# Kernel optimization log

Hardware: AMD Instinct MI355X
Metric: run time of the kernel (lower is better)

## Reference

```python
import jax, jax.numpy as jnp
import numpy as np

K = 128      # classes
CIN = 128    # ch_in
CL = 128     # ch_latent
B, H, W = 8, 1, 8192
SLOPE = 0.01 # F.leaky_relu default
EPS = 1e-5   # BatchNorm eps


def lrelu(x):
    return jnp.where(x >= 0, x, SLOPE * x)


def conv1x1(x, w, b):
    # x: (B,C,H,W), w: (O,C), b: (O,)
    return jnp.einsum('bchw,oc->bohw', x, w) + b[None, :, None, None]


def bn_eval(x, gamma, beta, mean, var):
    scale = gamma * jax.lax.rsqrt(var + EPS)
    return x * scale[None, :, None, None] + (beta - mean * scale)[None, :, None, None]


def setup_inputs() -> dict:
    key = jax.random.key(0)
    ks = jax.random.split(key, 16)
    def w(k, shape, fan_in):
        return jax.random.normal(k, shape, jnp.float32) / np.sqrt(fan_in)
    return {
        'x_in': jax.random.normal(ks[0], (B, CIN, H, W), jnp.float32),
        'cl1_w': w(ks[1], (CL, CIN), CIN), 'cl1_b': jnp.zeros((CL,), jnp.float32),
        'bn1_gamma': jnp.ones((CL,), jnp.float32), 'bn1_beta': jnp.zeros((CL,), jnp.float32),
        'bn1_mean': 0.1 * jax.random.normal(ks[2], (CL,), jnp.float32),
        'bn1_var': jax.random.uniform(ks[3], (CL,), jnp.float32, 0.5, 1.5),
        'cl2_w': w(ks[4], (CL, CL), CL), 'cl2_b': jnp.zeros((CL,), jnp.float32),
        'cl3_w': w(ks[5], (K + 1, CL), CL), 'cl3_b': jnp.zeros((K + 1,), jnp.float32),
        'reg1_w': w(ks[6], (CL, CIN), CIN), 'reg1_b': jnp.zeros((CL,), jnp.float32),
        'bnr_gamma': jnp.ones((CL,), jnp.float32), 'bnr_beta': jnp.zeros((CL,), jnp.float32),
        'bnr_mean': 0.1 * jax.random.normal(ks[7], (CL,), jnp.float32),
        'bnr_var': jax.random.uniform(ks[8], (CL,), jnp.float32, 0.5, 1.5),
        'cm2_w': w(ks[9], (K, CL, 32), CL), 'cm2_b': jnp.zeros((K, 32), jnp.float32),
        'cm3_w': w(ks[10], (K, 32, 1), 32), 'cm3_b': jnp.zeros((K, 1), jnp.float32),
    }


def reference(x_in, cl1_w, cl1_b, bn1_gamma, bn1_beta, bn1_mean, bn1_var,
              cl2_w, cl2_b, cl3_w, cl3_b,
              reg1_w, reg1_b, bnr_gamma, bnr_beta, bnr_mean, bnr_var,
              cm2_w, cm2_b, cm3_w, cm3_b):
    # classification branch
    x = lrelu(bn_eval(conv1x1(x_in, cl1_w, cl1_b), bn1_gamma, bn1_beta, bn1_mean, bn1_var))
    x = lrelu(conv1x1(x, cl2_w, cl2_b))
    x = conv1x1(x, cl3_w, cl3_b)                    # (B, K+1, H, W)
    logits = x[:, :K]
    mask = lrelu(x[:, -1:])                          # (B,1,H,W)
    inds = jnp.argmax(logits, axis=1)                # (B,H,W) int
    inds_r = inds.reshape(-1).astype(jnp.int32)      # (N,)
    xr = lrelu(bn_eval(conv1x1(x_in, reg1_w, reg1_b), bnr_gamma, bnr_beta, bnr_mean, bnr_var))
    # torch: transpose(1,3).reshape(-1, C)  -> (B,W,H,C) flatten
    xr = jnp.transpose(xr, (0, 3, 2, 1)).reshape(-1, CL)   # (N, CL)
    # CondMul 1: per-pixel gathered weight (N,CL,32)
    h = lrelu(jnp.einsum('ni,nio->no', xr, cm2_w[inds_r]) + cm2_b[inds_r])
    # CondMul 2: (N,32)->(N,1)
    reg = jnp.einsum('ni,nio->no', h, cm3_w[inds_r]) + cm3_b[inds_r]
    reg = reg.reshape(B, 1, 1, -1)                   # (B,1,1,H*W)
    x_real = (inds[:, None].astype(jnp.float32) + reg) * (1.0 / K)
    return x_real, mask
```

## Files before the change

### kernel.cpp

```cpp
#include <hip/hip_runtime.h>
#include <math.h>

#define NPOS 65536
#define NCH  128
#define DELTA 0.008f
#define HPAD 16

#define OFF_XR   0u
#define OFF_W1T  8388608u
#define OFF_W2T  (OFF_W1T + 16384u)
#define OFF_W3T  (OFF_W2T + 16384u)
#define OFF_B1F  (OFF_W3T + 16384u)
#define OFF_BRF  (OFF_B1F + 128u)
#define OFF_B2F  (OFF_BRF + 128u)
#define OFF_B3F  (OFF_B2F + 128u)
#define OFF_BF16 (OFF_B3F + 132u)
#define OFF_INT  (OFF_BF16 + 329728u)

#define UW1H 0u
#define UW1L 16384u
#define UWRH 32768u
#define UWRL 49152u
#define UW2H 65536u
#define UW2L 81920u
#define UW3H 98304u
#define UW3L 116736u
#define UW2K 135168u

#define NST 2080

typedef short bf16x8 __attribute__((ext_vector_type(8)));
typedef float f32x4 __attribute__((ext_vector_type(4)));
#define MFMA16 __builtin_amdgcn_mfma_f32_16x16x32_bf16

__device__ __forceinline__ float lrelu(float v) { return v >= 0.0f ? v : 0.01f * v; }
__device__ __forceinline__ unsigned short f2bf(float f) {
    unsigned u = __float_as_uint(f);
    return (unsigned short)((u + 0x7fffu + ((u >> 16) & 1u)) >> 16);
}
__device__ __forceinline__ float bf2f(unsigned short h) {
    return __uint_as_float(((unsigned)h) << 16);
}
__device__ __forceinline__ unsigned long long pack4(unsigned short a, unsigned short b,
                                                    unsigned short c, unsigned short d) {
    return (unsigned long long)a | ((unsigned long long)b << 16)
         | ((unsigned long long)c << 32) | ((unsigned long long)d << 48);
}

__global__ void k_prep(const float* __restrict__ cl1_w, const float* __restrict__ cl1_b,
                       const float* __restrict__ g1, const float* __restrict__ be1,
                       const float* __restrict__ mu1, const float* __restrict__ va1,
                       const float* __restrict__ cl2_w, const float* __restrict__ cl2_b,
                       const float* __restrict__ cl3_w, const float* __restrict__ cl3_b,
                       const float* __restrict__ reg1_w, const float* __restrict__ reg1_b,
                       const float* __restrict__ gr, const float* __restrict__ ber,
                       const float* __restrict__ mur, const float* __restrict__ var_,
                       const float* __restrict__ cm2w,
                       float* __restrict__ ws_f, unsigned short* __restrict__ wbf,
                       int* __restrict__ hist, int* __restrict__ cur,
                       int* __restrict__ fixcnt)
{
    const int bid = blockIdx.x;
    const int t = threadIdx.x;
    if (bid >= 128) {
        __shared__ float tl[32 * 132];
        int k = bid - 128;
        #pragma unroll
        for (int i = 0; i < 32; ++i) {
            float v = cm2w[(unsigned)k * 4096u + i * 128 + t];
            int ci = i * 4 + (t >> 5), o = t & 31;
            tl[o * 132 + ci] = v;
        }
        __syncthreads();
        #pragma unroll
        for (int i = 0; i < 32; ++i)
            wbf[UW2K + (unsigned)k * 4096u + i * 128 + t] = f2bf(tl[i * 132 + t]);
        return;
    }
    const int cout = bid;
    const int cin = t;
    const int row = cout * 128 + cin;
    float s1 = g1[cout] / sqrtf(va1[cout] + 1e-5f);
    float sr = gr[cout] / sqrtf(var_[cout] + 1e-5f);
    float w1 = cl1_w[row] * s1;
    float wr = reg1_w[row] * sr;
    float w2 = cl2_w[row];
    float w3 = cl3_w[row];
    ws_f[OFF_W1T + cin * 128 + cout] = w1;
    ws_f[OFF_W2T + cin * 128 + cout] = w2;
    ws_f[OFF_W3T + cin * 128 + cout] = w3;
    unsigned short h;
    h = f2bf(w1); wbf[UW1H + row] = h; wbf[UW1L + row] = f2bf(w1 - bf2f(h));
    h = f2bf(wr); wbf[UWRH + row] = h; wbf[UWRL + row] = f2bf(wr - bf2f(h));
    h = f2bf(w2); wbf[UW2H + row] = h; wbf[UW2L + row] = f2bf(w2 - bf2f(h));
    h = f2bf(w3); wbf[UW3H + row] = h; wbf[UW3L + row] = f2bf(w3 - bf2f(h));
    if (bid < 16) {
        float v = (bid == 0) ? cl3_w[128 * 128 + t] : 0.0f;
        int jj = (128 + bid) * 128 + t;
        h = f2bf(v); wbf[UW3H + jj] = h; wbf[UW3L + jj] = f2bf(v - bf2f(h));
    }
    if (bid == 0) {
        float s1b = g1[t] / sqrtf(va1[t] + 1e-5f);
        float srb = gr[t] / sqrtf(var_[t] + 1e-5f);
        ws_f[OFF_B1F + t] = cl1_b[t] * s1b + be1[t] - mu1[t] * s1b;
        ws_f[OFF_BRF + t] = reg1_b[t] * srb + ber[t] - mur[t] * srb;
        ws_f[OFF_B2F + t] = cl2_b[t];
        ws_f[OFF_B3F + t] = cl3_b[t];
        hist[t * HPAD] = 0;
        cur[t * HPAD] = 0;
    }
    if (bid == 1 && t == 0) { ws_f[OFF_B3F + 128] = cl3_b[128]; fixcnt[0] = 0; }
}

__global__ __launch_bounds__(256, 4)
void k_fused(const float* __restrict__ X, const float* __restrict__ wsf,
             const unsigned short* __restrict__ wbf,
             unsigned short* __restrict__ XRB, float* __restrict__ out_mask,
             int* __restrict__ inds, int* __restrict__ hist,
             int* __restrict__ fixcnt, int* __restrict__ fixlist)
{
    __shared__ __align__(16) unsigned short XBh[64 * 136];
    __shared__ __align__(16) unsigned short XBl[64 * 136];
    __shared__ float sm1[4 * 64];
    __shared__ float sm2[4 * 64];
    __shared__ int   si1[4 * 64];
    __shared__ int   lh[128];

    const int t = threadIdx.x;
    const int lane = t & 63;
    const int cl16 = lane & 15;
    const int q8 = (lane >> 4) * 8;
    const int q4 = (lane >> 4) * 4;
    const int wv = __builtin_amdgcn_readfirstlane(t >> 6);
    const unsigned nt64 = blockIdx.x * 64u;
    const unsigned base = nt64 + (nt64 >> 13) * 1040384u;

    const unsigned short* W1H = wbf + UW1H; const unsigned short* W1L = wbf + UW1L;
    const unsigned short* WRH = wbf + UWRH; const unsigned short* WRL = wbf + UWRL;
    const unsigned short* W2H = wbf + UW2H; const unsigned short* W2L = wbf + UW2L;
    const unsigned short* W3H = wbf + UW3H; const unsigned short* W3L = wbf + UW3L;
    const float* b1f = wsf + OFF_B1F;
    const float* brf = wsf + OFF_BRF;
    const float* b2f = wsf + OFF_B2F;
    const float* b3f = wsf + OFF_B3F;

    const f32x4 vzero = {0.f, 0.f, 0.f, 0.f};

    {
        const int pos = t & 63, cig = t >> 6;
        #pragma unroll
        for (int l = 0; l < 8; ++l) {
            int ci0 = cig * 32 + l * 4;
            float v0 = X[base + (unsigned)(ci0 + 0) * 8192u + pos];
            float v1 = X[base + (unsigned)(ci0 + 1) * 8192u + pos];
            float v2 = X[base + (unsigned)(ci0 + 2) * 8192u + pos];
            float v3 = X[base + (unsigned)(ci0 + 3) * 8192u + pos];
            unsigned short h0 = f2bf(v0), h1 = f2bf(v1), h2 = f2bf(v2), h3 = f2bf(v3);
            unsigned long long ph = pack4(h0, h1, h2, h3);
            unsigned long long pl = pack4(f2bf(v0 - bf2f(h0)), f2bf(v1 - bf2f(h1)),
                                          f2bf(v2 - bf2f(h2)), f2bf(v3 - bf2f(h3)));
            *(unsigned long long*)&XBh[pos * 136 + ci0] = ph;
            *(unsigned long long*)&XBl[pos * 136 + ci0] = pl;
        }
    }
    __syncthreads();

    f32x4 acc[2][4];

    #pragma unroll
    for (int m = 0; m < 2; ++m)
        #pragma unroll
        for (int n = 0; n < 4; ++n) acc[m][n] = vzero;
    #pragma unroll
    for (int kt = 0; kt < 4; ++kt) {
        bf16x8 Bh[4], Bl[4];
        #pragma unroll
        for (int n = 0; n < 4; ++n) {
            int bo = (n * 16 + cl16) * 136 + kt * 32 + q8;
            Bh[n] = *(const bf16x8*)&XBh[bo];
            Bl[n] = *(const bf16x8*)&XBl[bo];
        }
        #pragma unroll
        for (int m = 0; m < 2; ++m) {
            int ao = (wv * 32 + m * 16 + cl16) * 128 + kt * 32 + q8;
            bf16x8 arh = *(const bf16x8*)&WRH[ao], arl = *(const bf16x8*)&WRL[ao];
            #pragma unroll
            for (int n = 0; n < 4; ++n) {
                acc[m][n] = MFMA16(arh, Bl[n], acc[m][n], 0, 0, 0);
                acc[m][n] = MFMA16(arl, Bh[n], acc[m][n], 0, 0, 0);
                acc[m][n] = MFMA16(arh, Bh[n], acc[m][n], 0, 0, 0);
            }
        }
    }
    {
        #pragma unroll
        for (int m = 0; m < 2; ++m) {
            int cb = wv * 32 + m * 16 + q4;
            float br0 = brf[cb], br1 = brf[cb + 1], br2 = brf[cb + 2], br3 = brf[cb + 3];
            #pragma unroll
            for (int n = 0; n < 4; ++n) {
                unsigned pb = (nt64 + n * 16 + cl16) * 128u + cb;
                ushort4 xo;
                xo.x = f2bf(lrelu(acc[m][n][0] + br0));
                xo.y = f2bf(lrelu(acc[m][n][1] + br1));
                xo.z = f2bf(lrelu(acc[m][n][2] + br2));
                xo.w = f2bf(lrelu(acc[m][n][3] + br3));
                *(ushort4*)&XRB[pb] = xo;
            }
        }
    }

    #pragma unroll
    for (int m = 0; m < 2; ++m)
        #pragma unroll
        for (int n = 0; n < 4; ++n) acc[m][n] = vzero;
    #pragma unroll
    for (int kt = 0; kt < 4; ++kt) {
        bf16x8 Bh[4], Bl[4];
        #pragma unroll
        for (int n = 0; n < 4; ++n) {
            int bo = (n * 16 + cl16) * 136 + kt * 32 + q8;
            Bh[n] = *(const bf16x8*)&XBh[bo];
            Bl[n] = *(const bf16x8*)&XBl[bo];
        }
        #pragma unroll
        for (int m = 0; m < 2; ++m) {
            int ao = (wv * 32 + m * 16 + cl16) * 128 + kt * 32 + q8;
            bf16x8 a1h = *(const bf16x8*)&W1H[ao], a1l = *(const bf16x8*)&W1L[ao];
            #pragma unroll
            for (int n = 0; n < 4; ++n) {
                acc[m][n] = MFMA16(a1h, Bl[n], acc[m][n], 0, 0, 0);
                acc[m][n] = MFMA16(a1l, Bh[n], acc[m][n], 0, 0, 0);
                acc[m][n] = MFMA16(a1h, Bh[n], acc[m][n], 0, 0, 0);
            }
        }
    }
    __syncthreads();
    {
        #pragma unroll
        for (int m = 0; m < 2; ++m) {
            int cb = wv * 32 + m * 16 + q4;
            float b0 = b1f[cb], b1 = b1f[cb + 1], b2 = b1f[cb + 2], b3 = b1f[cb + 3];
            #pragma unroll
            for (int n = 0; n < 4; ++n) {
                float v0 = lrelu(acc[m][n][0] + b0), v1 = lrelu(acc[m][n][1] + b1);
                float v2 = lrelu(acc[m][n][2] + b2), v3 = lrelu(acc[m][n][3] + b3);
                unsigned short h0 = f2bf(v0), h1 = f2bf(v1), h2 = f2bf(v2), h3 = f2bf(v3);
                unsigned long long ph = pack4(h0, h1, h2, h3);
                unsigned long long pl = pack4(f2bf(v0 - bf2f(h0)), f2bf(v1 - bf2f(h1)),
                                              f2bf(v2 - bf2f(h2)), f2bf(v3 - bf2f(h3)));
                int idx = (n * 16 + cl16) * 136 + cb;
                *(unsigned long long*)&XBh[idx] = ph;
                *(unsigned long long*)&XBl[idx] = pl;
            }
        }
    }
    __syncthreads();

    #pragma unroll
    for (int m = 0; m < 2; ++m)
        #pragma unroll
        for (int n = 0; n < 4; ++n) acc[m][n] = vzero;
    #pragma unroll
    for (int kt = 0; kt < 4; ++kt) {
        bf16x8 Bh[4], Bl[4];
        #pragma unroll
        for (int n = 0; n < 4; ++n) {
            int bo = (n * 16 + cl16) * 136 + kt * 32 + q8;
            Bh[n] = *(const bf16x8*)&XBh[bo];
            Bl[n] = *(const bf16x8*)&XBl[bo];
        }
        #pragma unroll
        for (int m = 0; m < 2; ++m) {
            int ao = (wv * 32 + m * 16 + cl16) * 128 + kt * 32 + q8;
            bf16x8 ah = *(const bf16x8*)&W2H[ao], al = *(const bf16x8*)&W2L[ao];
            #pragma unroll
            for (int n = 0; n < 4; ++n) {
                acc[m][n] = MFMA16(ah, Bl[n], acc[m][n], 0, 0, 0);
                acc[m][n] = MFMA16(al, Bh[n], acc[m][n], 0, 0, 0);
                acc[m][n] = MFMA16(ah, Bh[n], acc[m][n], 0, 0, 0);
            }
        }
    }
    __syncthreads();
    {
        #pragma unroll
        for (int m = 0; m < 2; ++m) {
            int cb = wv * 32 + m * 16 + q4;
            float b0 = b2f[cb], b1 = b2f[cb + 1], b2 = b2f[cb + 2], b3 = b2f[cb + 3];
            #pragma unroll
            for (int n = 0; n < 4; ++n) {
                float v0 = lrelu(acc[m][n][0] + b0), v1 = lrelu(acc[m][n][1] + b1);
                float v2 = lrelu(acc[m][n][2] + b2), v3 = lrelu(acc[m][n][3] + b3);
                unsigned short h0 = f2bf(v0), h1 = f2bf(v1), h2 = f2bf(v2), h3 = f2bf(v3);
                unsigned long long ph = pack4(h0, h1, h2, h3);
                unsigned long long pl = pack4(f2bf(v0 - bf2f(h0)), f2bf(v1 - bf2f(h1)),
                                              f2bf(v2 - bf2f(h2)), f2bf(v3 - bf2f(h3)));
                int idx = (n * 16 + cl16) * 136 + cb;
                *(unsigned long long*)&XBh[idx] = ph;
                *(unsigned long long*)&XBl[idx] = pl;
            }
        }
    }
    __syncthreads();

    f32x4 accM = vzero;
    #pragma unroll
    for (int m = 0; m < 2; ++m)
        #pragma unroll
        for (int n = 0; n < 4; ++n) acc[m][n] = vzero;
    #pragma unroll
    for (int kt = 0; kt < 4; ++kt) {
        bf16x8 Bh[4], Bl[4];
        #pragma unroll
        for (int n = 0; n < 4; ++n) {
            int bo = (n * 16 + cl16) * 136 + kt * 32 + q8;
            Bh[n] = *(const bf16x8*)&XBh[bo];
            Bl[n] = *(const bf16x8*)&XBl[bo];
        }
        #pragma unroll
        for (int m = 0; m < 2; ++m) {
            int ao = (wv * 32 + m * 16 + cl16) * 128 + kt * 32 + q8;
            bf16x8 ah = *(const bf16x8*)&W3H[ao], al = *(const bf16x8*)&W3L[ao];
            #pragma unroll
            for (int n = 0; n < 4; ++n) {
                acc[m][n] = MFMA16(ah, Bl[n], acc[m][n], 0, 0, 0);
                acc[m][n] = MFMA16(al, Bh[n], acc[m][n], 0, 0, 0);
                acc[m][n] = MFMA16(ah, Bh[n], acc[m][n], 0, 0, 0);
            }
        }
        {
            int boM = (wv * 16 + cl16) * 136 + kt * 32 + q8;
            bf16x8 BhM = *(const bf16x8*)&XBh[boM];
            bf16x8 BlM = *(const bf16x8*)&XBl[boM];
            int ao = (128 + cl16) * 128 + kt * 32 + q8;
            bf16x8 ah = *(const bf16x8*)&W3H[ao], al = *(const bf16x8*)&W3L[ao];
            accM = MFMA16(ah, BlM, accM, 0, 0, 0);
            accM = MFMA16(al, BhM, accM, 0, 0, 0);
            accM = MFMA16(ah, BhM, accM, 0, 0, 0);
        }
    }

    {
        float bb[2][4];
        #pragma unroll
        for (int m = 0; m < 2; ++m) {
            int cb = wv * 32 + m * 16 + q4;
            bb[m][0] = b3f[cb]; bb[m][1] = b3f[cb + 1];
            bb[m][2] = b3f[cb + 2]; bb[m][3] = b3f[cb + 3];
        }
        float m1[4], m2[4]; int i1[4];
        #pragma unroll
        for (int n = 0; n < 4; ++n) {
            m1[n] = -1e30f; m2[n] = -1e30f; i1[n] = 0;
            #pragma unroll
            for (int m = 0; m < 2; ++m) {
                int cb = wv * 32 + m * 16 + q4;
                #pragma unroll
                for (int r = 0; r < 4; ++r) {
                    float v = acc[m][n][r] + bb[m][r];
                    if (v > m1[n]) { m2[n] = m1[n]; m1[n] = v; i1[n] = cb + r; }
                    else if (v > m2[n]) m2[n] = v;
                }
            }
        }
        #pragma unroll
        for (int off = 16; off <= 32; off <<= 1) {
            #pragma unroll
            for (int n = 0; n < 4; ++n) {
                float om1 = __shfl_xor(m1[n], off);
                float om2 = __shfl_xor(m2[n], off);
                int   oi1 = __shfl_xor(i1[n], off);
                if (om1 > m1[n] || (om1 == m1[n] && oi1 < i1[n])) {
                    m2[n] = fmaxf(m1[n], om2); m1[n] = om1; i1[n] = oi1;
                } else {
                    m2[n] = fmaxf(m2[n], om1);
                }
            }
        }
        if ((lane >> 4) == 0) {
            #pragma unroll
            for (int n = 0; n < 4; ++n) {
                sm1[wv * 64 + n * 16 + cl16] = m1[n];
                sm2[wv * 64 + n * 16 + cl16] = m2[n];
                si1[wv * 64 + n * 16 + cl16] = i1[n];
            }
        }
    }
    if ((lane >> 4) == 0) {
        float mb = b3f[128];
        out_mask[nt64 + wv * 16 + cl16] = lrelu(accM[0] + mb);
    }
    if (t < 128) lh[t] = 0;
    __syncthreads();
    if (t < 64) {
        float m1 = sm1[t], m2 = sm2[t];
        int i1 = si1[t];
        #pragma unroll
        for (int w = 1; w < 4; ++w) {
            float v1 = sm1[w * 64 + t];
            float v2 = sm2[w * 64 + t];
            int   vi = si1[w * 64 + t];
            if (v1 > m1) { m2 = fmaxf(m1, v2); m1 = v1; i1 = vi; }
            else         { m2 = fmaxf(m2, v1); }
        }
        int n = nt64 + t;
        inds[n] = i1;
        atomicAdd(&lh[i1], 1);
        if (m1 - m2 < DELTA) {
            int slot = atomicAdd(fixcnt, 1);
            fixlist[slot] = n;
        }
    }
    __syncthreads();
    if (t < 128 && lh[t] > 0) atomicAdd(&hist[t * HPAD], lh[t]);
}

__global__ __launch_bounds__(256, 4)
void k_fix(const float* __restrict__ X, const float* __restrict__ wsf,
           const int* __restrict__ fixcnt, const int* __restrict__ fixlist,
           int* __restrict__ inds, int* __restrict__ hist)
{
    __shared__ float xw[4][128];
    const int cnt = fixcnt[0];
    const int t = threadIdx.x;
    const int lane = t & 63;
    const int wv = t >> 6;
    const float* W1T = wsf + OFF_W1T;
    const float* W2T = wsf + OFF_W2T;
    const float* W3T = wsf + OFF_W3T;
    const float* b1f = wsf + OFF_B1F;
    const float* b2f = wsf + OFF_B2F;
    const float* b3f = wsf + OFF_B3F;

    for (int idx = blockIdx.x * 4 + wv; idx < cnt; idx += 2048) {
        int n = fixlist[idx];
        int oldid = inds[n];
        const float* xb = X + (unsigned)(n >> 13) * 1048576u + (unsigned)(n & 8191);
        float x0 = xb[(unsigned)lane * 8192u];
        float x1 = xb[(unsigned)(64 + lane) * 8192u];
        float a0, a1;

        xw[wv][lane] = x0; xw[wv][64 + lane] = x1;
        a0 = 0.f; a1 = 0.f;
        #pragma unroll 16
        for (int ci = 0; ci < 128; ++ci) {
            float xv = xw[wv][ci];
            const float* wr = W1T + ci * 128;
            a0 = fmaf(wr[lane], xv, a0);
            a1 = fmaf(wr[64 + lane], xv, a1);
        }
        x0 = lrelu(a0 + b1f[lane]); x1 = lrelu(a1 + b1f[64 + lane]);

        xw[wv][lane] = x0; xw[wv][64 + lane] = x1;
        a0 = 0.f; a1 = 0.f;
        #pragma unroll 16
        for (int ci = 0; ci < 128; ++ci) {
            float xv = xw[wv][ci];
            const float* wr = W2T + ci * 128;
            a0 = fmaf(wr[lane], xv, a0);
            a1 = fmaf(wr[64 + lane], xv, a1);
        }
        x0 = lrelu(a0 + b2f[lane]); x1 = lrelu(a1 + b2f[64 + lane]);

        xw[wv][lane] = x0; xw[wv][64 + lane] = x1;
        a0 = 0.f; a1 = 0.f;
        #pragma unroll 16
        for (int ci = 0; ci < 128; ++ci) {
            float xv = xw[wv][ci];
            const float* wr = W3T + ci * 128;
            a0 = fmaf(wr[lane], xv, a0);
            a1 = fmaf(wr[64 + lane], xv, a1);
        }
        float L0 = a0 + b3f[lane], L1 = a1 + b3f[64 + lane];
        float v; int id;
        if (L0 >= L1) { v = L0; id = lane; } else { v = L1; id = 64 + lane; }
        #pragma unroll
        for (int off = 1; off < 64; off <<= 1) {
            float ov = __shfl_xor(v, off);
            int   oi = __shfl_xor(id, off);
            if (ov > v || (ov == v && oi < id)) { v = ov; id = oi; }
        }
        if (lane == 0 && id != oldid) {
            inds[n] = id;
            atomicSub(&hist[oldid * HPAD], 1);
            atomicAdd(&hist[id * HPAD], 1);
        }
    }
}

__global__ void k_scatter(const int* __restrict__ inds, const int* __restrict__ hist,
                          int* __restrict__ cur, int* __restrict__ bucket)
{
    __shared__ int lh[128];
    __shared__ int gb[128];
    __shared__ int sv[128];
    __shared__ int sh[128];
    int t = threadIdx.x;
    if (t < 128) { int h = hist[t * HPAD]; sh[t] = h; sv[t] = h; lh[t] = 0; }
    __syncthreads();
    for (int d = 1; d < 128; d <<= 1) {
        int a = (t < 128 && t >= d) ? sv[t - d] : 0;
        __syncthreads();
        if (t < 128) sv[t] += a;
        __syncthreads();
    }
    int n = blockIdx.x * 256 + t;
    int id = inds[n];
    int r = atomicAdd(&lh[id], 1);
    __syncthreads();
    if (t < 128 && lh[t] > 0)
        gb[t] = (sv[t] - sh[t]) + atomicAdd(&cur[t * HPAD], lh[t]);
    __syncthreads();
    bucket[gb[id] + r] = n;
}

__global__ __launch_bounds__(256, 4)
void k_reg(const unsigned short* __restrict__ XRB, const unsigned short* __restrict__ wbf,
           const float* __restrict__ cm2b, const float* __restrict__ cm3w,
           const float* __restrict__ cm3b, const int* __restrict__ hist,
           const int* __restrict__ bucket, float* __restrict__ out)
{
    __shared__ __align__(16) unsigned short XP[4 * NST];
    __shared__ float red[64];
    __shared__ int sh[128];
    __shared__ int sv[128];
    __shared__ int st[128];
    __shared__ int skj[2];
    int bid = blockIdx.x;
    int t = threadIdx.x;
    if (t < 128) {
        int h = hist[t * HPAD];
        sh[t] = h; sv[t] = h; st[t] = (h + 63) >> 6;
    }
    __syncthreads();
    for (int d = 1; d < 128; d <<= 1) {
        int a = (t < 128 && t >= d) ? sv[t - d] : 0;
        int b = (t < 128 && t >= d) ? st[t - d] : 0;
        __syncthreads();
        if (t < 128) { sv[t] += a; st[t] += b; }
        __syncthreads();
    }
    if (bid >= st[127]) return;
    if (t < 128) {
        int ntk = (sh[t] + 63) >> 6;
        int tb = st[t] - ntk;
        if (bid >= tb && bid < st[t]) { skj[0] = t; skj[1] = bid - tb; }
    }
    __syncthreads();
    const int k = skj[0];
    const int start = skj[1] << 6;
    const int cnt = sh[k];
    const int base = sv[k] - sh[k];
    int lane = t & 63;
    int wv = __builtin_amdgcn_readfirstlane(t >> 6);
    const int n16 = lane & 15;
    const int quad = lane >> 4;

    {
        int rs = t >> 2;
        int q = t & 3;
        int sidx = start + rs;
        if (sidx >= cnt) sidx = cnt - 1;
        int n = bucket[base + sidx];
        const uint4* src = (const uint4*)(XRB + (unsigned)n * 128u + q * 32);
        uint4 a0 = src[0], a1 = src[1], a2 = src[2], a3 = src[3];
        unsigned db = (rs >> 4) * NST + q * 512 + (rs & 15) * 8;
        *(uint4*)&XP[db]       = a0;
        *(uint4*)&XP[db + 128] = a1;
        *(uint4*)&XP[db + 256] = a2;
        *(uint4*)&XP[db + 384] = a3;
    }
    __syncthreads();

    const unsigned short* wb = wbf + UW2K + (unsigned)k * 4096u;
    bf16x8 Bf[2][4];
    #pragma unroll
    for (int nf = 0; nf < 2; ++nf)
        #pragma unroll
        for (int kt = 0; kt < 4; ++kt)
            Bf[nf][kt] = *(const bf16x8*)&wb[(nf * 16 + n16) * 128 + kt * 32 + quad * 8];

    const f32x4 vzero = {0.f, 0.f, 0.f, 0.f};
    f32x4 acc[2];
    acc[0] = vzero; acc[1] = vzero;
    #pragma unroll
    for (int kt = 0; kt < 4; ++kt) {
        bf16x8 Af = *(const bf16x8*)&XP[wv * NST + kt * 512 + lane * 8];
        #pragma unroll
        for (int nf = 0; nf < 2; ++nf)
            acc[nf] = MFMA16(Af, Bf[nf][kt], acc[nf], 0, 0, 0);
    }

    float b2a = cm2b[k * 32 + n16], b2b = cm2b[k * 32 + 16 + n16];
    float w3a = cm3w[k * 32 + n16], w3b = cm3w[k * 32 + 16 + n16];
    #pragma unroll
    for (int r = 0; r < 4; ++r) {
        float p = lrelu(acc[0][r] + b2a) * w3a
                + lrelu(acc[1][r] + b2b) * w3b;
        p += __shfl_xor(p, 1);
        p += __shfl_xor(p, 2);
        p += __shfl_xor(p, 4);
        p += __shfl_xor(p, 8);
        if (n16 == 0)
            red[wv * 16 + quad * 4 + r] = p;
    }
    __syncthreads();
    if (t < 64 && start + t < cnt) {
        int n2 = bucket[base + start + t];
        out[n2] = ((float)k + red[t] + cm3b[k]) * (1.0f / 128.0f);
    }
}

extern "C" void kernel_launch(void* const* d_in, const int* in_sizes, int n_in,
                              void* d_out, int out_size, void* d_ws, size_t ws_size,
                              hipStream_t stream)
{
    (void)in_sizes; (void)n_in; (void)out_size; (void)ws_size;
    const float* x_in   = (const float*)d_in[0];
    const float* cl1_w  = (const float*)d_in[1];
    const float* cl1_b  = (const float*)d_in[2];
    const float* g1     = (const float*)d_in[3];
    const float* be1    = (const float*)d_in[4];
    const float* mu1    = (const float*)d_in[5];
    const float* va1    = (const float*)d_in[6];
    const float* cl2_w  = (const float*)d_in[7];
    const float* cl2_b  = (const float*)d_in[8];
    const float* cl3_w  = (const float*)d_in[9];
    const float* cl3_b  = (const float*)d_in[10];
    const float* reg1_w = (const float*)d_in[11];
    const float* reg1_b = (const float*)d_in[12];
    const float* gr     = (const float*)d_in[13];
    const float* ber    = (const float*)d_in[14];
    const float* mur    = (const float*)d_in[15];
    const float* var_   = (const float*)d_in[16];
    const float* cm2w   = (const float*)d_in[17];
    const float* cm2b   = (const float*)d_in[18];
    const float* cm3w   = (const float*)d_in[19];
    const float* cm3b   = (const float*)d_in[20];

    float* ws_f = (float*)d_ws;
    unsigned short* XRB = (unsigned short*)(ws_f + OFF_XR);
    unsigned short* wbf = (unsigned short*)(ws_f + OFF_BF16);
    int*   wsi    = (int*)(ws_f + OFF_INT);
    int*   inds   = wsi;
    int*   hist   = inds + 65536;
    int*   offb   = hist + 2048;
    int*   cur    = offb + 128;
    int*   ntt    = cur + 2048;
    int*   fixcnt = ntt + 4;
    int*   tiles  = fixcnt + 4;
    int*   fixlist= tiles + 1536;
    int*   bucket = fixlist + 65536;
    float* out = (float*)d_out;

    hipLaunchKernelGGL(k_prep, dim3(256), dim3(128), 0, stream,
                       cl1_w, cl1_b, g1, be1, mu1, va1, cl2_w, cl2_b, cl3_w, cl3_b,
                       reg1_w, reg1_b, gr, ber, mur, var_, cm2w, ws_f, wbf, hist, cur,
                       fixcnt);
    hipLaunchKernelGGL(k_fused, dim3(1024), dim3(256), 0, stream,
                       x_in, ws_f, wbf, XRB, out + 65536, inds, hist, fixcnt, fixlist);
    hipLaunchKernelGGL(k_fix, dim3(512), dim3(256), 0, stream,
                       x_in, ws_f, fixcnt, fixlist, inds, hist);
    hipLaunchKernelGGL(k_scatter, dim3(256), dim3(256), 0, stream,
                       inds, hist, cur, bucket);
    hipLaunchKernelGGL(k_reg, dim3(1536), dim3(256), 0, stream,
                       XRB, wbf, cm2b, cm3w, cm3b, hist, bucket, out);
}
```

Measured before the change: 204.0 us.

## Merge five kernel launches into one persistent kernel with grid barriers

Replaces the prep, fused, fix, scatter and regression kernels with a single 1024-block kernel that runs each stage in turn, separated by a hierarchical atomic grid barrier. Stage shared memory is overlaid through a union, and the regression stage loops over tiles so it fits the fixed grid. The aim is to remove per-launch overhead and the idle gaps between the small dependent kernels. In exchange it relies on all 1024 blocks being resident at once to avoid deadlock, adds barrier spin cost, and needs an extra memset before the launch.

```diff
diff --git a/kernel.cpp b/kernel.cpp
--- a/kernel.cpp
+++ b/kernel.cpp
@@ -47,568 +47,586 @@
          | ((unsigned long long)c << 32) | ((unsigned long long)d << 48);
 }
 
-__global__ void k_prep(const float* __restrict__ cl1_w, const float* __restrict__ cl1_b,
-                       const float* __restrict__ g1, const float* __restrict__ be1,
-                       const float* __restrict__ mu1, const float* __restrict__ va1,
-                       const float* __restrict__ cl2_w, const float* __restrict__ cl2_b,
-                       const float* __restrict__ cl3_w, const float* __restrict__ cl3_b,
-                       const float* __restrict__ reg1_w, const float* __restrict__ reg1_b,
-                       const float* __restrict__ gr, const float* __restrict__ ber,
-                       const float* __restrict__ mur, const float* __restrict__ var_,
-                       const float* __restrict__ cm2w,
-                       float* __restrict__ ws_f, unsigned short* __restrict__ wbf,
-                       int* __restrict__ hist, int* __restrict__ cur,
-                       int* __restrict__ fixcnt)
+__device__ __forceinline__ void gridbar(int* cnt, int* root, int* gen, int bargen)
 {
-    const int bid = blockIdx.x;
-    const int t = threadIdx.x;
-    if (bid >= 128) {
-        __shared__ float tl[32 * 132];
-        int k = bid - 128;
-        #pragma unroll
-        for (int i = 0; i < 32; ++i) {
-            float v = cm2w[(unsigned)k * 4096u + i * 128 + t];
-            int ci = i * 4 + (t >> 5), o = t & 31;
-            tl[o * 132 + ci] = v;
-        }
-        __syncthreads();
-        #pragma unroll
-        for (int i = 0; i < 32; ++i)
-            wbf[UW2K + (unsigned)k * 4096u + i * 128 + t] = f2bf(tl[i * 132 + t]);
-        return;
-    }
-    const int cout = bid;
-    const int cin = t;
-    const int row = cout * 128 + cin;
-    float s1 = g1[cout] / sqrtf(va1[cout] + 1e-5f);
-    float sr = gr[cout] / sqrtf(var_[cout] + 1e-5f);
-    float w1 = cl1_w[row] * s1;
-    float wr = reg1_w[row] * sr;
-    float w2 = cl2_w[row];
-    float w3 = cl3_w[row];
-    ws_f[OFF_W1T + cin * 128 + cout] = w1;
-    ws_f[OFF_W2T + cin * 128 + cout] = w2;
-    ws_f[OFF_W3T + cin * 128 + cout] = w3;
-    unsigned short h;
-    h = f2bf(w1); wbf[UW1H + row] = h; wbf[UW1L + row] = f2bf(w1 - bf2f(h));
-    h = f2bf(wr); wbf[UWRH + row] = h; wbf[UWRL + row] = f2bf(wr - bf2f(h));
-    h = f2bf(w2); wbf[UW2H + row] = h; wbf[UW2L + row] = f2bf(w2 - bf2f(h));
-    h = f2bf(w3); wbf[UW3H + row] = h; wbf[UW3L + row] = f2bf(w3 - bf2f(h));
-    if (bid < 16) {
-        float v = (bid == 0) ? cl3_w[128 * 128 + t] : 0.0f;
-        int jj = (128 + bid) * 128 + t;
-        h = f2bf(v); wbf[UW3H + jj] = h; wbf[UW3L + jj] = f2bf(v - bf2f(h));
-    }
-    if (bid == 0) {
-        float s1b = g1[t] / sqrtf(va1[t] + 1e-5f);
-        float srb = gr[t] / sqrtf(var_[t] + 1e-5f);
-        ws_f[OFF_B1F + t] = cl1_b[t] * s1b + be1[t] - mu1[t] * s1b;
-        ws_f[OFF_BRF + t] = reg1_b[t] * srb + ber[t] - mur[t] * srb;
-        ws_f[OFF_B2F + t] = cl2_b[t];
-        ws_f[OFF_B3F + t] = cl3_b[t];
-        hist[t * HPAD] = 0;
-        cur[t * HPAD] = 0;
-    }
-    if (bid == 1 && t == 0) { ws_f[OFF_B3F + 128] = cl3_b[128]; fixcnt[0] = 0; }
-}
-
-__global__ __launch_bounds__(256, 4)
-void k_fused(const float* __restrict__ X, const float* __restrict__ wsf,
-             const unsigned short* __restrict__ wbf,
-             unsigned short* __restrict__ XRB, float* __restrict__ out_mask,
-             int* __restrict__ inds, int* __restrict__ hist,
-             int* __restrict__ fixcnt, int* __restrict__ fixlist)
-{
-    __shared__ __align__(16) unsigned short XBh[64 * 136];
-    __shared__ __align__(16) unsigned short XBl[64 * 136];
-    __shared__ float sm1[4 * 64];
-    __shared__ float sm2[4 * 64];
-    __shared__ int   si1[4 * 64];
-    __shared__ int   lh[128];
-
-    const int t = threadIdx.x;
-    const int lane = t & 63;
-    const int cl16 = lane & 15;
-    const int q8 = (lane >> 4) * 8;
-    const int q4 = (lane >> 4) * 4;
-    const int wv = __builtin_amdgcn_readfirstlane(t >> 6);
-    const unsigned nt64 = blockIdx.x * 64u;
-    const unsigned base = nt64 + (nt64 >> 13) * 1040384u;
-
-    const unsigned short* W1H = wbf + UW1H; const unsigned short* W1L = wbf + UW1L;
-    const unsigned short* WRH = wbf + UWRH; const unsigned short* WRL = wbf + UWRL;
-    const unsigned short* W2H = wbf + UW2H; const unsigned short* W2L = wbf + UW2L;
-    const unsigned short* W3H = wbf + UW3H; const unsigned short* W3L = wbf + UW3L;
-    const float* b1f = wsf + OFF_B1F;
-    const float* brf = wsf + OFF_BRF;
-    const float* b2f = wsf + OFF_B2F;
-    const float* b3f = wsf + OFF_B3F;
-
-    const f32x4 vzero = {0.f, 0.f, 0.f, 0.f};
-
-    {
-        const int pos = t & 63, cig = t >> 6;
-        #pragma unroll
-        for (int l = 0; l < 8; ++l) {
-            int ci0 = cig * 32 + l * 4;
-            float v0 = X[base + (unsigned)(ci0 + 0) * 8192u + pos];
-            float v1 = X[base + (unsigned)(ci0 + 1) * 8192u + pos];
-            float v2 = X[base + (unsigned)(ci0 + 2) * 8192u + pos];
-            float v3 = X[base + (unsigned)(ci0 + 3) * 8192u + pos];
-            unsigned short h0 = f2bf(v0), h1 = f2bf(v1), h2 = f2bf(v2), h3 = f2bf(v3);
-            unsigned long long ph = pack4(h0, h1, h2, h3);
-            unsigned long long pl = pack4(f2bf(v0 - bf2f(h0)), f2bf(v1 - bf2f(h1)),
-                                          f2bf(v2 - bf2f(h2)), f2bf(v3 - bf2f(h3)));
-            *(unsigned long long*)&XBh[pos * 136 + ci0] = ph;
-            *(unsigned long long*)&XBl[pos * 136 + ci0] = pl;
-        }
+    __syncthreads();
+    if (threadIdx.x == 0) {
+        __threadfence();
+        int grp = (int)(blockIdx.x & 31u);
+        if (atomicAdd(&cnt[grp * HPAD], 1) == 32 * bargen - 1) {
+            if (atomicAdd(root, 1) == 32 * bargen - 1) {
+                __hip_atomic_store(gen, bargen, __ATOMIC_RELEASE,
+                                   __HIP_MEMORY_SCOPE_AGENT);
+            }
+        }
+        while (__hip_atomic_load(gen, __ATOMIC_ACQUIRE,
+                                 __HIP_MEMORY_SCOPE_AGENT) < bargen)
+            __builtin_amdgcn_s_sleep(8);
+        __threadfence();
     }
     __syncthreads();
-
-    f32x4 acc[2][4];
-
-    #pragma unroll
-    for (int m = 0; m < 2; ++m)
-        #pragma unroll
-        for (int n = 0; n < 4; ++n) acc[m][n] = vzero;
-    #pragma unroll
-    for (int kt = 0; kt < 4; ++kt) {
-        bf16x8 Bh[4], Bl[4];
-        #pragma unroll
-        for (int n = 0; n < 4; ++n) {
-            int bo = (n * 16 + cl16) * 136 + kt * 32 + q8;
-            Bh[n] = *(const bf16x8*)&XBh[bo];
-            Bl[n] = *(const bf16x8*)&XBl[bo];
-        }
-        #pragma unroll
-        for (int m = 0; m < 2; ++m) {
-            int ao = (wv * 32 + m * 16 + cl16) * 128 + kt * 32 + q8;
-            bf16x8 arh = *(const bf16x8*)&WRH[ao], arl = *(const bf16x8*)&WRL[ao];
-            #pragma unroll
-            for (int n = 0; n < 4; ++n) {
-                acc[m][n] = MFMA16(arh, Bl[n], acc[m][n], 0, 0, 0);
-                acc[m][n] = MFMA16(arl, Bh[n], acc[m][n], 0, 0, 0);
-                acc[m][n] = MFMA16(arh, Bh[n], acc[m][n], 0, 0, 0);
-            }
+}
+
+__global__ __launch_bounds__(256, 4)
+void k_mega(const float* __restrict__ X,
+            const float* __restrict__ cl1_w, const float* __restrict__ cl1_b,
+            const float* __restrict__ g1, const float* __restrict__ be1,
+            const float* __restrict__ mu1, const float* __restrict__ va1,
+            const float* __restrict__ cl2_w, const float* __restrict__ cl2_b,
+            const float* __restrict__ cl3_w, const float* __restrict__ cl3_b,
+            const float* __restrict__ reg1_w, const float* __restrict__ reg1_b,
+            const float* __restrict__ gr, const float* __restrict__ ber,
+            const float* __restrict__ mur, const float* __restrict__ var_,
+            const float* __restrict__ cm2w, const float* __restrict__ cm2b,
+            const float* __restrict__ cm3w, const float* __restrict__ cm3b,
+            float* __restrict__ wsf, unsigned short* __restrict__ wbf,
+            unsigned short* __restrict__ XRB, float* __restrict__ out_mask,
+            int* __restrict__ inds, int* __restrict__ hist, int* __restrict__ cur,
+            int* __restrict__ fixcnt, int* __restrict__ fixlist,
+            int* __restrict__ bucket, float* __restrict__ out,
+            int* __restrict__ bcnt, int* __restrict__ broot, int* __restrict__ bgen)
+{
+    __shared__ union __align__(16) SM {
+        struct { float tl[32 * 132]; } prep;
+        struct {
+            unsigned short XBh[64 * 136];
+            unsigned short XBl[64 * 136];
+            float sm1[256]; float sm2[256]; int si1[256];
+            int lh[128];
+        } f;
+        struct { float xw[4][128]; } x;
+        struct { int lh[128]; int gb[128]; int sv[128]; int sh[128]; } s;
+        struct {
+            unsigned short XP[4 * NST];
+            float red[64];
+            int sh[128]; int sv[128]; int st[128]; int skj[2];
+        } r;
+    } U;
+
+    const int t = threadIdx.x;
+    const int bid0 = blockIdx.x;
+    const int lane = t & 63;
+    const int wv = __builtin_amdgcn_readfirstlane(t >> 6);
+
+    if (bid0 < 128) {
+        if (t < 128) {
+            const int cout = bid0;
+            const int cin = t;
+            const int row = cout * 128 + cin;
+            float s1 = g1[cout] / sqrtf(va1[cout] + 1e-5f);
+            float sr = gr[cout] / sqrtf(var_[cout] + 1e-5f);
+            float w1 = cl1_w[row] * s1;
+            float wr = reg1_w[row] * sr;
+            float w2 = cl2_w[row];
+            float w3 = cl3_w[row];
+            wsf[OFF_W1T + cin * 128 + cout] = w1;
+            wsf[OFF_W2T + cin * 128 + cout] = w2;
+            wsf[OFF_W3T + cin * 128 + cout] = w3;
+            unsigned short h;
+            h = f2bf(w1); wbf[UW1H + row] = h; wbf[UW1L + row] = f2bf(w1 - bf2f(h));
+            h = f2bf(wr); wbf[UWRH + row] = h; wbf[UWRL + row] = f2bf(wr - bf2f(h));
+            h = f2bf(w2); wbf[UW2H + row] = h; wbf[UW2L + row] = f2bf(w2 - bf2f(h));
+            h = f2bf(w3); wbf[UW3H + row] = h; wbf[UW3L + row] = f2bf(w3 - bf2f(h));
+            if (bid0 < 16) {
+                float v = (bid0 == 0) ? cl3_w[128 * 128 + t] : 0.0f;
+                int jj = (128 + bid0) * 128 + t;
+                h = f2bf(v); wbf[UW3H + jj] = h; wbf[UW3L + jj] = f2bf(v - bf2f(h));
+            }
+            if (bid0 == 0) {
+                float s1b = g1[t] / sqrtf(va1[t] + 1e-5f);
+                float srb = gr[t] / sqrtf(var_[t] + 1e-5f);
+                wsf[OFF_B1F + t] = cl1_b[t] * s1b + be1[t] - mu1[t] * s1b;
+                wsf[OFF_BRF + t] = reg1_b[t] * srb + ber[t] - mur[t] * srb;
+                wsf[OFF_B2F + t] = cl2_b[t];
+                wsf[OFF_B3F + t] = cl3_b[t];
+                hist[t * HPAD] = 0;
+                cur[t * HPAD] = 0;
+            }
+            if (bid0 == 1 && t == 0) { wsf[OFF_B3F + 128] = cl3_b[128]; fixcnt[0] = 0; }
+        }
+    } else if (bid0 < 256) {
+        int k = bid0 - 128;
+        if (t < 128) {
+            #pragma unroll
+            for (int i = 0; i < 32; ++i) {
+                float v = cm2w[(unsigned)k * 4096u + i * 128 + t];
+                int ci = i * 4 + (t >> 5), o = t & 31;
+                U.prep.tl[o * 132 + ci] = v;
+            }
+        }
+        __syncthreads();
+        if (t < 128) {
+            #pragma unroll
+            for (int i = 0; i < 32; ++i)
+                wbf[UW2K + (unsigned)k * 4096u + i * 128 + t] = f2bf(U.prep.tl[i * 132 + t]);
         }
     }
+    gridbar(bcnt, broot, bgen, 1);
+
     {
-        #pragma unroll
-        for (int m = 0; m < 2; ++m) {
-            int cb = wv * 32 + m * 16 + q4;
-            float br0 = brf[cb], br1 = brf[cb + 1], br2 = brf[cb + 2], br3 = brf[cb + 3];
-            #pragma unroll
-            for (int n = 0; n < 4; ++n) {
-                unsigned pb = (nt64 + n * 16 + cl16) * 128u + cb;
-                ushort4 xo;
-                xo.x = f2bf(lrelu(acc[m][n][0] + br0));
-                xo.y = f2bf(lrelu(acc[m][n][1] + br1));
-                xo.z = f2bf(lrelu(acc[m][n][2] + br2));
-                xo.w = f2bf(lrelu(acc[m][n][3] + br3));
-                *(ushort4*)&XRB[pb] = xo;
-            }
-        }
-    }
-
-    #pragma unroll
-    for (int m = 0; m < 2; ++m)
-        #pragma unroll
-        for (int n = 0; n < 4; ++n) acc[m][n] = vzero;
-    #pragma unroll
-    for (int kt = 0; kt < 4; ++kt) {
-        bf16x8 Bh[4], Bl[4];
-        #pragma unroll
-        for (int n = 0; n < 4; ++n) {
-            int bo = (n * 16 + cl16) * 136 + kt * 32 + q8;
-            Bh[n] = *(const bf16x8*)&XBh[bo];
-            Bl[n] = *(const bf16x8*)&XBl[bo];
-        }
-        #pragma unroll
-        for (int m = 0; m < 2; ++m) {
-            int ao = (wv * 32 + m * 16 + cl16) * 128 + kt * 32 + q8;
-            bf16x8 a1h = *(const bf16x8*)&W1H[ao], a1l = *(const bf16x8*)&W1L[ao];
-            #pragma unroll
-            for (int n = 0; n < 4; ++n) {
-                acc[m][n] = MFMA16(a1h, Bl[n], acc[m][n], 0, 0, 0);
-                acc[m][n] = MFMA16(a1l, Bh[n], acc[m][n], 0, 0, 0);
-                acc[m][n] = MFMA16(a1h, Bh[n], acc[m][n], 0, 0, 0);
-            }
-        }
-    }
-    __syncthreads();
-    {
-        #pragma unroll
-        for (int m = 0; m < 2; ++m) {
-            int cb = wv * 32 + m * 16 + q4;
-            float b0 = b1f[cb], b1 = b1f[cb + 1], b2 = b1f[cb + 2], b3 = b1f[cb + 3];
-            #pragma unroll
-            for (int n = 0; n < 4; ++n) {
-                float v0 = lrelu(acc[m][n][0] + b0), v1 = lrelu(acc[m][n][1] + b1);
-                float v2 = lrelu(acc[m][n][2] + b2), v3 = lrelu(acc[m][n][3] + b3);
+        auto& XBh = U.f.XBh;  auto& XBl = U.f.XBl;
+        auto& sm1 = U.f.sm1;  auto& sm2 = U.f.sm2;  auto& si1 = U.f.si1;
+        auto& lh  = U.f.lh;
+
+        const int cl16 = lane & 15;
+        const int q8 = (lane >> 4) * 8;
+        const int q4 = (lane >> 4) * 4;
+        const unsigned nt64 = bid0 * 64u;
+        const unsigned base = nt64 + (nt64 >> 13) * 1040384u;
+
+        const unsigned short* W1H = wbf + UW1H; const unsigned short* W1L = wbf + UW1L;
+        const unsigned short* WRH = wbf + UWRH; const unsigned short* WRL = wbf + UWRL;
+        const unsigned short* W2H = wbf + UW2H; const unsigned short* W2L = wbf + UW2L;
+        const unsigned short* W3H = wbf + UW3H; const unsigned short* W3L = wbf + UW3L;
+        const float* b1f = wsf + OFF_B1F;
+        const float* brf = wsf + OFF_BRF;
+        const float* b2f = wsf + OFF_B2F;
+        const float* b3f = wsf + OFF_B3F;
+
+        const f32x4 vzero = {0.f, 0.f, 0.f, 0.f};
+
+        {
+            const int pos = t & 63, cig = t >> 6;
+            #pragma unroll
+            for (int l = 0; l < 8; ++l) {
+                int ci0 = cig * 32 + l * 4;
+                float v0 = X[base + (unsigned)(ci0 + 0) * 8192u + pos];
+                float v1 = X[base + (unsigned)(ci0 + 1) * 8192u + pos];
+                float v2 = X[base + (unsigned)(ci0 + 2) * 8192u + pos];
+                float v3 = X[base + (unsigned)(ci0 + 3) * 8192u + pos];
                 unsigned short h0 = f2bf(v0), h1 = f2bf(v1), h2 = f2bf(v2), h3 = f2bf(v3);
                 unsigned long long ph = pack4(h0, h1, h2, h3);
                 unsigned long long pl = pack4(f2bf(v0 - bf2f(h0)), f2bf(v1 - bf2f(h1)),
                                               f2bf(v2 - bf2f(h2)), f2bf(v3 - bf2f(h3)));
-                int idx = (n * 16 + cl16) * 136 + cb;
-                *(unsigned long long*)&XBh[idx] = ph;
-                *(unsigned long long*)&XBl[idx] = pl;
-            }
-        }
+                *(unsigned long long*)&XBh[pos * 136 + ci0] = ph;
+                *(unsigned long long*)&XBl[pos * 136 + ci0] = pl;
+            }
+        }
+        __syncthreads();
+
+        f32x4 acc[2][4];
+
+        #pragma unroll
+        for (int m = 0; m < 2; ++m)
+            #pragma unroll
+            for (int n = 0; n < 4; ++n) acc[m][n] = vzero;
+        #pragma unroll
+        for (int kt = 0; kt < 4; ++kt) {
+            bf16x8 Bh[4], Bl[4];
+            #pragma unroll
+            for (int n = 0; n < 4; ++n) {
+                int bo = (n * 16 + cl16) * 136 + kt * 32 + q8;
+                Bh[n] = *(const bf16x8*)&XBh[bo];
+                Bl[n] = *(const bf16x8*)&XBl[bo];
+            }
+            #pragma unroll
+            for (int m = 0; m < 2; ++m) {
+                int ao = (wv * 32 + m * 16 + cl16) * 128 + kt * 32 + q8;
+                bf16x8 arh = *(const bf16x8*)&WRH[ao], arl = *(const bf16x8*)&WRL[ao];
+                #pragma unroll
+                for (int n = 0; n < 4; ++n) {
+                    acc[m][n] = MFMA16(arh, Bl[n], acc[m][n], 0, 0, 0);
+                    acc[m][n] = MFMA16(arl, Bh[n], acc[m][n], 0, 0, 0);
+                    acc[m][n] = MFMA16(arh, Bh[n], acc[m][n], 0, 0, 0);
+                }
+            }
+        }
+        {
+            #pragma unroll
+            for (int m = 0; m < 2; ++m) {
+                int cb = wv * 32 + m * 16 + q4;
+                float br0 = brf[cb], br1 = brf[cb + 1], br2 = brf[cb + 2], br3 = brf[cb + 3];
+                #pragma unroll
+                for (int n = 0; n < 4; ++n) {
+                    unsigned pb = (nt64 + n * 16 + cl16) * 128u + cb;
+                    ushort4 xo;
+                    xo.x = f2bf(lrelu(acc[m][n][0] + br0));
+                    xo.y = f2bf(lrelu(acc[m][n][1] + br1));
+                    xo.z = f2bf(lrelu(acc[m][n][2] + br2));
+                    xo.w = f2bf(lrelu(acc[m][n][3] + br3));
+                    *(ushort4*)&XRB[pb] = xo;
+                }
+            }
+        }
+
+        #pragma unroll
+        for (int m = 0; m < 2; ++m)
+            #pragma unroll
+            for (int n = 0; n < 4; ++n) acc[m][n] = vzero;
+        #pragma unroll
+        for (int kt = 0; kt < 4; ++kt) {
+            bf16x8 Bh[4], Bl[4];
+            #pragma unroll
+            for (int n = 0; n < 4; ++n) {
+                int bo = (n * 16 + cl16) * 136 + kt * 32 + q8;
+                Bh[n] = *(const bf16x8*)&XBh[bo];
+                Bl[n] = *(const bf16x8*)&XBl[bo];
+            }
+            #pragma unroll
+            for (int m = 0; m < 2; ++m) {
+                int ao = (wv * 32 + m * 16 + cl16) * 128 + kt * 32 + q8;
+                bf16x8 a1h = *(const bf16x8*)&W1H[ao], a1l = *(const bf16x8*)&W1L[ao];
+                #pragma unroll
+                for (int n = 0; n < 4; ++n) {
+                    acc[m][n] = MFMA16(a1h, Bl[n], acc[m][n], 0, 0, 0);
+                    acc[m][n] = MFMA16(a1l, Bh[n], acc[m][n], 0, 0, 0);
+                    acc[m][n] = MFMA16(a1h, Bh[n], acc[m][n], 0, 0, 0);
+                }
+            }
+        }
+        __syncthreads();
+        {
+            #pragma unroll
+            for (int m = 0; m < 2; ++m) {
+                int cb = wv * 32 + m * 16 + q4;
+                float b0 = b1f[cb], b1 = b1f[cb + 1], b2 = b1f[cb + 2], b3 = b1f[cb + 3];
+                #pragma unroll
+                for (int n = 0; n < 4; ++n) {
+                    float v0 = lrelu(acc[m][n][0] + b0), v1 = lrelu(acc[m][n][1] + b1);
+                    float v2 = lrelu(acc[m][n][2] + b2), v3 = lrelu(acc[m][n][3] + b3);
+                    unsigned short h0 = f2bf(v0), h1 = f2bf(v1), h2 = f2bf(v2), h3 = f2bf(v3);
+                    unsigned long long ph = pack4(h0, h1, h2, h3);
+                    unsigned long long pl = pack4(f2bf(v0 - bf2f(h0)), f2bf(v1 - bf2f(h1)),
+                                                  f2bf(v2 - bf2f(h2)), f2bf(v3 - bf2f(h3)));
+                    int idx = (n * 16 + cl16) * 136 + cb;
+                    *(unsigned long long*)&XBh[idx] = ph;
+                    *(unsigned long long*)&XBl[idx] = pl;
+                }
+            }
+        }
+        __syncthreads();
+
+        #pragma unroll
+        for (int m = 0; m < 2; ++m)
+            #pragma unroll
+            for (int n = 0; n < 4; ++n) acc[m][n] = vzero;
+        #pragma unroll
+        for (int kt = 0; kt < 4; ++kt) {
+            bf16x8 Bh[4], Bl[4];
+            #pragma unroll
+            for (int n = 0; n < 4; ++n) {
+                int bo = (n * 16 + cl16) * 136 + kt * 32 + q8;
+                Bh[n] = *(const bf16x8*)&XBh[bo];
+                Bl[n] = *(const bf16x8*)&XBl[bo];
+            }
+            #pragma unroll
+            for (int m = 0; m < 2; ++m) {
+                int ao = (wv * 32 + m * 16 + cl16) * 128 + kt * 32 + q8;
+                bf16x8 ah = *(const bf16x8*)&W2H[ao], al = *(const bf16x8*)&W2L[ao];
+                #pragma unroll
+                for (int n = 0; n < 4; ++n) {
+                    acc[m][n] = MFMA16(ah, Bl[n], acc[m][n], 0, 0, 0);
+                    acc[m][n] = MFMA16(al, Bh[n], acc[m][n], 0, 0, 0);
+                    acc[m][n] = MFMA16(ah, Bh[n], acc[m][n], 0, 0, 0);
+                }
+            }
+        }
+        __syncthreads();
+        {
+            #pragma unroll
+            for (int m = 0; m < 2; ++m) {
+                int cb = wv * 32 + m * 16 + q4;
+                float b0 = b2f[cb], b1 = b2f[cb + 1], b2 = b2f[cb + 2], b3 = b2f[cb + 3];
+                #pragma unroll
+                for (int n = 0; n < 4; ++n) {
+                    float v0 = lrelu(acc[m][n][0] + b0), v1 = lrelu(acc[m][n][1] + b1);
+                    float v2 = lrelu(acc[m][n][2] + b2), v3 = lrelu(acc[m][n][3] + b3);
+                    unsigned short h0 = f2bf(v0), h1 = f2bf(v1), h2 = f2bf(v2), h3 = f2bf(v3);
+                    unsigned long long ph = pack4(h0, h1, h2, h3);
+                    unsigned long long pl = pack4(f2bf(v0 - bf2f(h0)), f2bf(v1 - bf2f(h1)),
+                                                  f2bf(v2 - bf2f(h2)), f2bf(v3 - bf2f(h3)));
+                    int idx = (n * 16 + cl16) * 136 + cb;
+                    *(unsigned long long*)&XBh[idx] = ph;
+                    *(unsigned long long*)&XBl[idx] = pl;
+                }
+            }
+        }
+        __syncthreads();
+
+        f32x4 accM = vzero;
+        #pragma unroll
+        for (int m = 0; m < 2; ++m)
+            #pragma unroll
+            for (int n = 0; n < 4; ++n) acc[m][n] = vzero;
+        #pragma unroll
+        for (int kt = 0; kt < 4; ++kt) {
+            bf16x8 Bh[4], Bl[4];
+            #pragma unroll
+            for (int n = 0; n < 4; ++n) {
+                int bo = (n * 16 + cl16) * 136 + kt * 32 + q8;
+                Bh[n] = *(const bf16x8*)&XBh[bo];
+                Bl[n] = *(const bf16x8*)&XBl[bo];
+            }
+            #pragma unroll
+            for (int m = 0; m < 2; ++m) {
+                int ao = (wv * 32 + m * 16 + cl16) * 128 + kt * 32 + q8;
+                bf16x8 ah = *(const bf16x8*)&W3H[ao], al = *(const bf16x8*)&W3L[ao];
+                #pragma unroll
+                for (int n = 0; n < 4; ++n) {
+                    acc[m][n] = MFMA16(ah, Bl[n], acc[m][n], 0, 0, 0);
+                    acc[m][n] = MFMA16(al, Bh[n], acc[m][n], 0, 0, 0);
+                    acc[m][n] = MFMA16(ah, Bh[n], acc[m][n], 0, 0, 0);
+                }
+            }
+            {
+                int boM = (wv * 16 + cl16) * 136 + kt * 32 + q8;
+                bf16x8 BhM = *(const bf16x8*)&XBh[boM];
+                bf16x8 BlM = *(const bf16x8*)&XBl[boM];
+                int ao = (128 + cl16) * 128 + kt * 32 + q8;
+                bf16x8 ah = *(const bf16x8*)&W3H[ao], al = *(const bf16x8*)&W3L[ao];
+                accM = MFMA16(ah, BlM, accM, 0, 0, 0);
+                accM = MFMA16(al, BhM, accM, 0, 0, 0);
+                accM = MFMA16(ah, BhM, accM, 0, 0, 0);
+            }
+        }
+
+        {
+            float bb[2][4];
+            #pragma unroll
+            for (int m = 0; m < 2; ++m) {
+                int cb = wv * 32 + m * 16 + q4;
+                bb[m][0] = b3f[cb]; bb[m][1] = b3f[cb + 1];
+                bb[m][2] = b3f[cb + 2]; bb[m][3] = b3f[cb + 3];
+            }
+            float m1[4], m2[4]; int i1[4];
+            #pragma unroll
+            for (int n = 0; n < 4; ++n) {
+                m1[n] = -1e30f; m2[n] = -1e30f; i1[n] = 0;
+                #pragma unroll
+                for (int m = 0; m < 2; ++m) {
+                    int cb = wv * 32 + m * 16 + q4;
+                    #pragma unroll
+                    for (int r = 0; r < 4; ++r) {
+                        float v = acc[m][n][r] + bb[m][r];
+                        if (v > m1[n]) { m2[n] = m1[n]; m1[n] = v; i1[n] = cb + r; }
+                        else if (v > m2[n]) m2[n] = v;
+                    }
+                }
+            }
+            #pragma unroll
+            for (int off = 16; off <= 32; off <<= 1) {
+                #pragma unroll
+                for (int n = 0; n < 4; ++n) {
+                    float om1 = __shfl_xor(m1[n], off);
+                    float om2 = __shfl_xor(m2[n], off);
+                    int   oi1 = __shfl_xor(i1[n], off);
+                    if (om1 > m1[n] || (om1 == m1[n] && oi1 < i1[n])) {
+                        m2[n] = fmaxf(m1[n], om2); m1[n] = om1; i1[n] = oi1;
+                    } else {
+                        m2[n] = fmaxf(m2[n], om1);
+                    }
+                }
+            }
+            if ((lane >> 4) == 0) {
+                #pragma unroll
+                for (int n = 0; n < 4; ++n) {
+                    sm1[wv * 64 + n * 16 + cl16] = m1[n];
+                    sm2[wv * 64 + n * 16 + cl16] = m2[n];
+                    si1[wv * 64 + n * 16 + cl16] = i1[n];
+                }
+            }
+        }
+        if ((lane >> 4) == 0) {
+            float mb = b3f[128];
+            out_mask[nt64 + wv * 16 + cl16] = lrelu(accM[0] + mb);
+        }
+        if (t < 128) lh[t] = 0;
+        __syncthreads();
+        if (t < 64) {
+            float m1 = sm1[t], m2 = sm2[t];
+            int i1 = si1[t];
+            #pragma unroll
+            for (int w = 1; w < 4; ++w) {
+                float v1 = sm1[w * 64 + t];
+                float v2 = sm2[w * 64 + t];
+                int   vi = si1[w * 64 + t];
+                if (v1 > m1) { m2 = fmaxf(m1, v2); m1 = v1; i1 = vi; }
+                else         { m2 = fmaxf(m2, v1); }
+            }
+            int n = nt64 + t;
+            inds[n] = i1;
+            atomicAdd(&lh[i1], 1);
+            if (m1 - m2 < DELTA) {
+                int slot = atomicAdd(fixcnt, 1);
+                fixlist[slot] = n;
+            }
+        }
+        __syncthreads();
+        if (t < 128 && lh[t] > 0) atomicAdd(&hist[t * HPAD], lh[t]);
     }
-    __syncthreads();
-
-    #pragma unroll
-    for (int m = 0; m < 2; ++m)
-        #pragma unroll
-        for (int n = 0; n < 4; ++n) acc[m][n] = vzero;
-    #pragma unroll
-    for (int kt = 0; kt < 4; ++kt) {
-        bf16x8 Bh[4], Bl[4];
-        #pragma unroll
-        for (int n = 0; n < 4; ++n) {
-            int bo = (n * 16 + cl16) * 136 + kt * 32 + q8;
-            Bh[n] = *(const bf16x8*)&XBh[bo];
-            Bl[n] = *(const bf16x8*)&XBl[bo];
-        }
-        #pragma unroll
-        for (int m = 0; m < 2; ++m) {
-            int ao = (wv * 32 + m * 16 + cl16) * 128 + kt * 32 + q8;
-            bf16x8 ah = *(const bf16x8*)&W2H[ao], al = *(const bf16x8*)&W2L[ao];
-            #pragma unroll
-            for (int n = 0; n < 4; ++n) {
-                acc[m][n] = MFMA16(ah, Bl[n], acc[m][n], 0, 0, 0);
-                acc[m][n] = MFMA16(al, Bh[n], acc[m][n], 0, 0, 0);
-                acc[m][n] = MFMA16(ah, Bh[n], acc[m][n], 0, 0, 0);
+    gridbar(bcnt, broot, bgen, 2);
+
+    {
+        const int cnt = fixcnt[0];
+        const float* W1T = wsf + OFF_W1T;
+        const float* W2T = wsf + OFF_W2T;
+        const float* W3T = wsf + OFF_W3T;
+        const float* b1f = wsf + OFF_B1F;
+        const float* b2f = wsf + OFF_B2F;
+        const float* b3f = wsf + OFF_B3F;
+
+        for (int idx = bid0 * 4 + wv; idx < cnt; idx += 4096) {
+            int n = fixlist[idx];
+            int oldid = inds[n];
+            const float* xb = X + (unsigned)(n >> 13) * 1048576u + (unsigned)(n & 8191);
+            float x0 = xb[(unsigned)lane * 8192u];
+            float x1 = xb[(unsigned)(64 + lane) * 8192u];
+            float a0, a1;
+
+            U.x.xw[wv][lane] = x0; U.x.xw[wv][64 + lane] = x1;
+            a0 = 0.f; a1 = 0.f;
+            #pragma unroll 16
+            for (int ci = 0; ci < 128; ++ci) {
+                float xv = U.x.xw[wv][ci];
+                const float* wr = W1T + ci * 128;
+                a0 = fmaf(wr[lane], xv, a0);
+                a1 = fmaf(wr[64 + lane], xv, a1);
+            }
+            x0 = lrelu(a0 + b1f[lane]); x1 = lrelu(a1 + b1f[64 + lane]);
+
+            U.x.xw[wv][lane] = x0; U.x.xw[wv][64 + lane] = x1;
+            a0 = 0.f; a1 = 0.f;
+            #pragma unroll 16
+            for (int ci = 0; ci < 128; ++ci) {
+                float xv = U.x.xw[wv][ci];
+                const float* wr = W2T + ci * 128;
+                a0 = fmaf(wr[lane], xv, a0);
+                a1 = fmaf(wr[64 + lane], xv, a1);
+            }
+            x0 = lrelu(a0 + b2f[lane]); x1 = lrelu(a1 + b2f[64 + lane]);
+
+            U.x.xw[wv][lane] = x0; U.x.xw[wv][64 + lane] = x1;
+            a0 = 0.f; a1 = 0.f;
+            #pragma unroll 16
+            for (int ci = 0; ci < 128; ++ci) {
+                float xv = U.x.xw[wv][ci];
+                const float* wr = W3T + ci * 128;
+                a0 = fmaf(wr[lane], xv, a0);
+                a1 = fmaf(wr[64 + lane], xv, a1);
+            }
+            float L0 = a0 + b3f[lane], L1 = a1 + b3f[64 + lane];
+            float v; int id;
+            if (L0 >= L1) { v = L0; id = lane; } else { v = L1; id = 64 + lane; }
+            #pragma unroll
+            for (int off = 1; off < 64; off <<= 1) {
+                float ov = __shfl_xor(v, off);
+                int   oi = __shfl_xor(id, off);
+                if (ov > v || (ov == v && oi < id)) { v = ov; id = oi; }
+            }
+            if (lane == 0 && id != oldid) {
+                inds[n] = id;
+                atomicSub(&hist[oldid * HPAD], 1);
+                atomicAdd(&hist[id * HPAD], 1);
             }
         }
     }
-    __syncthreads();
+    gridbar(bcnt, broot, bgen, 3);
+
+    if (bid0 < 256) {
+        if (t < 128) { int h = hist[t * HPAD]; U.s.sh[t] = h; U.s.sv[t] = h; U.s.lh[t] = 0; }
+        __syncthreads();
+        for (int d = 1; d < 128; d <<= 1) {
+            int a = (t < 128 && t >= d) ? U.s.sv[t - d] : 0;
+            __syncthreads();
+            if (t < 128) U.s.sv[t] += a;
+            __syncthreads();
+        }
+        int n = bid0 * 256 + t;
+        int id = inds[n];
+        int r = atomicAdd(&U.s.lh[id], 1);
+        __syncthreads();
+        if (t < 128 && U.s.lh[t] > 0)
+            U.s.gb[t] = (U.s.sv[t] - U.s.sh[t]) + atomicAdd(&cur[t * HPAD], U.s.lh[t]);
+        __syncthreads();
+        bucket[U.s.gb[id] + r] = n;
+    }
+    gridbar(bcnt, broot, bgen, 4);
+
     {
-        #pragma unroll
-        for (int m = 0; m < 2; ++m) {
-            int cb = wv * 32 + m * 16 + q4;
-            float b0 = b2f[cb], b1 = b2f[cb + 1], b2 = b2f[cb + 2], b3 = b2f[cb + 3];
-            #pragma unroll
-            for (int n = 0; n < 4; ++n) {
-                float v0 = lrelu(acc[m][n][0] + b0), v1 = lrelu(acc[m][n][1] + b1);
-                float v2 = lrelu(acc[m][n][2] + b2), v3 = lrelu(acc[m][n][3] + b3);
-                unsigned short h0 = f2bf(v0), h1 = f2bf(v1), h2 = f2bf(v2), h3 = f2bf(v3);
-                unsigned long long ph = pack4(h0, h1, h2, h3);
-                unsigned long long pl = pack4(f2bf(v0 - bf2f(h0)), f2bf(v1 - bf2f(h1)),
-                                              f2bf(v2 - bf2f(h2)), f2bf(v3 - bf2f(h3)));
-                int idx = (n * 16 + cl16) * 136 + cb;
-                *(unsigned long long*)&XBh[idx] = ph;
-                *(unsigned long long*)&XBl[idx] = pl;
-            }
-        }
-    }
-    __syncthreads();
-
-    f32x4 accM = vzero;
-    #pragma unroll
-    for (int m = 0; m < 2; ++m)
-        #pragma unroll
-        for (int n = 0; n < 4; ++n) acc[m][n] = vzero;
-    #pragma unroll
-    for (int kt = 0; kt < 4; ++kt) {
-        bf16x8 Bh[4], Bl[4];
-        #pragma unroll
-        for (int n = 0; n < 4; ++n) {
-            int bo = (n * 16 + cl16) * 136 + kt * 32 + q8;
-            Bh[n] = *(const bf16x8*)&XBh[bo];
-            Bl[n] = *(const bf16x8*)&XBl[bo];
-        }
-        #pragma unroll
-        for (int m = 0; m < 2; ++m) {
-            int ao = (wv * 32 + m * 16 + cl16) * 128 + kt * 32 + q8;
-            bf16x8 ah = *(const bf16x8*)&W3H[ao], al = *(const bf16x8*)&W3L[ao];
-            #pragma unroll
-            for (int n = 0; n < 4; ++n) {
-                acc[m][n] = MFMA16(ah, Bl[n], acc[m][n], 0, 0, 0);
-                acc[m][n] = MFMA16(al, Bh[n], acc[m][n], 0, 0, 0);
-                acc[m][n] = MFMA16(ah, Bh[n], acc[m][n], 0, 0, 0);
-            }
-        }
-        {
-            int boM = (wv * 16 + cl16) * 136 + kt * 32 + q8;
-            bf16x8 BhM = *(const bf16x8*)&XBh[boM];
-            bf16x8 BlM = *(const bf16x8*)&XBl[boM];
-            int ao = (128 + cl16) * 128 + kt * 32 + q8;
-            bf16x8 ah = *(const bf16x8*)&W3H[ao], al = *(const bf16x8*)&W3L[ao];
-            accM = MFMA16(ah, BlM, accM, 0, 0, 0);
-            accM = MFMA16(al, BhM, accM, 0, 0, 0);
-            accM = MFMA16(ah, BhM, accM, 0, 0, 0);
-        }
-    }
-
-    {
-        float bb[2][4];
-        #pragma unroll
-        for (int m = 0; m < 2; ++m) {
-            int cb = wv * 32 + m * 16 + q4;
-            bb[m][0] = b3f[cb]; bb[m][1] = b3f[cb + 1];
-            bb[m][2] = b3f[cb + 2]; bb[m][3] = b3f[cb + 3];
-        }
-        float m1[4], m2[4]; int i1[4];
-        #pragma unroll
-        for (int n = 0; n < 4; ++n) {
-            m1[n] = -1e30f; m2[n] = -1e30f; i1[n] = 0;
-            #pragma unroll
-            for (int m = 0; m < 2; ++m) {
-                int cb = wv * 32 + m * 16 + q4;
-                #pragma unroll
-                for (int r = 0; r < 4; ++r) {
-                    float v = acc[m][n][r] + bb[m][r];
-                    if (v > m1[n]) { m2[n] = m1[n]; m1[n] = v; i1[n] = cb + r; }
-                    else if (v > m2[n]) m2[n] = v;
-                }
-            }
-        }
-        #pragma unroll
-        for (int off = 16; off <= 32; off <<= 1) {
-            #pragma unroll
-            for (int n = 0; n < 4; ++n) {
-                float om1 = __shfl_xor(m1[n], off);
-                float om2 = __shfl_xor(m2[n], off);
-                int   oi1 = __shfl_xor(i1[n], off);
-                if (om1 > m1[n] || (om1 == m1[n] && oi1 < i1[n])) {
-                    m2[n] = fmaxf(m1[n], om2); m1[n] = om1; i1[n] = oi1;
-                } else {
-                    m2[n] = fmaxf(m2[n], om1);
-                }
-            }
-        }
-        if ((lane >> 4) == 0) {
-            #pragma unroll
-            for (int n = 0; n < 4; ++n) {
-                sm1[wv * 64 + n * 16 + cl16] = m1[n];
-                sm2[wv * 64 + n * 16 + cl16] = m2[n];
-                si1[wv * 64 + n * 16 + cl16] = i1[n];
-            }
-        }
-    }
-    if ((lane >> 4) == 0) {
-        float mb = b3f[128];
-        out_mask[nt64 + wv * 16 + cl16] = lrelu(accM[0] + mb);
-    }
-    if (t < 128) lh[t] = 0;
-    __syncthreads();
-    if (t < 64) {
-        float m1 = sm1[t], m2 = sm2[t];
-        int i1 = si1[t];
-        #pragma unroll
-        for (int w = 1; w < 4; ++w) {
-            float v1 = sm1[w * 64 + t];
-            float v2 = sm2[w * 64 + t];
-            int   vi = si1[w * 64 + t];
-            if (v1 > m1) { m2 = fmaxf(m1, v2); m1 = v1; i1 = vi; }
-            else         { m2 = fmaxf(m2, v1); }
-        }
-        int n = nt64 + t;
-        inds[n] = i1;
-        atomicAdd(&lh[i1], 1);
-        if (m1 - m2 < DELTA) {
-            int slot = atomicAdd(fixcnt, 1);
-            fixlist[slot] = n;
-        }
-    }
-    __syncthreads();
-    if (t < 128 && lh[t] > 0) atomicAdd(&hist[t * HPAD], lh[t]);
-}
-
-__global__ __launch_bounds__(256, 4)
-void k_fix(const float* __restrict__ X, const float* __restrict__ wsf,
-           const int* __restrict__ fixcnt, const int* __restrict__ fixlist,
-           int* __restrict__ inds, int* __restrict__ hist)
-{
-    __shared__ float xw[4][128];
-    const int cnt = fixcnt[0];
-    const int t = threadIdx.x;
-    const int lane = t & 63;
-    const int wv = t >> 6;
-    const float* W1T = wsf + OFF_W1T;
-    const float* W2T = wsf + OFF_W2T;
-    const float* W3T = wsf + OFF_W3T;
-    const float* b1f = wsf + OFF_B1F;
-    const float* b2f = wsf + OFF_B2F;
-    const float* b3f = wsf + OFF_B3F;
-
-    for (int idx = blockIdx.x * 4 + wv; idx < cnt; idx += 2048) {
-        int n = fixlist[idx];
-        int oldid = inds[n];
-        const float* xb = X + (unsigned)(n >> 13) * 1048576u + (unsigned)(n & 8191);
-        float x0 = xb[(unsigned)lane * 8192u];
-        float x1 = xb[(unsigned)(64 + lane) * 8192u];
-        float a0, a1;
-
-        xw[wv][lane] = x0; xw[wv][64 + lane] = x1;
-        a0 = 0.f; a1 = 0.f;
-        #pragma unroll 16
-        for (int ci = 0; ci < 128; ++ci) {
-            float xv = xw[wv][ci];
-            const float* wr = W1T + ci * 128;
-            a0 = fmaf(wr[lane], xv, a0);
-            a1 = fmaf(wr[64 + lane], xv, a1);
-        }
-        x0 = lrelu(a0 + b1f[lane]); x1 = lrelu(a1 + b1f[64 + lane]);
-
-        xw[wv][lane] = x0; xw[wv][64 + lane] = x1;
-        a0 = 0.f; a1 = 0.f;
-        #pragma unroll 16
-        for (int ci = 0; ci < 128; ++ci) {
-            float xv = xw[wv][ci];
-            const float* wr = W2T + ci * 128;
-            a0 = fmaf(wr[lane], xv, a0);
-            a1 = fmaf(wr[64 + lane], xv, a1);
-        }
-        x0 = lrelu(a0 + b2f[lane]); x1 = lrelu(a1 + b2f[64 + lane]);
-
-        xw[wv][lane] = x0; xw[wv][64 + lane] = x1;
-        a0 = 0.f; a1 = 0.f;
-        #pragma unroll 16
-        for (int ci = 0; ci < 128; ++ci) {
-            float xv = xw[wv][ci];
-            const float* wr = W3T + ci * 128;
-            a0 = fmaf(wr[lane], xv, a0);
-            a1 = fmaf(wr[64 + lane], xv, a1);
-        }
-        float L0 = a0 + b3f[lane], L1 = a1 + b3f[64 + lane];
-        float v; int id;
-        if (L0 >= L1) { v = L0; id = lane; } else { v = L1; id = 64 + lane; }
-        #pragma unroll
-        for (int off = 1; off < 64; off <<= 1) {
-            float ov = __shfl_xor(v, off);
-            int   oi = __shfl_xor(id, off);
-            if (ov > v || (ov == v && oi < id)) { v = ov; id = oi; }
-        }
-        if (lane == 0 && id != oldid) {
-            inds[n] = id;
-            atomicSub(&hist[oldid * HPAD], 1);
-            atomicAdd(&hist[id * HPAD], 1);
-        }
-    }
-}
-
-__global__ void k_scatter(const int* __restrict__ inds, const int* __restrict__ hist,
-                          int* __restrict__ cur, int* __restrict__ bucket)
-{
-    __shared__ int lh[128];
-    __shared__ int gb[128];
-    __shared__ int sv[128];
-    __shared__ int sh[128];
-    int t = threadIdx.x;
-    if (t < 128) { int h = hist[t * HPAD]; sh[t] = h; sv[t] = h; lh[t] = 0; }
-    __syncthreads();
-    for (int d = 1; d < 128; d <<= 1) {
-        int a = (t < 128 && t >= d) ? sv[t - d] : 0;
-        __syncthreads();
-        if (t < 128) sv[t] += a;
-        __syncthreads();
-    }
-    int n = blockIdx.x * 256 + t;
-    int id = inds[n];
-    int r = atomicAdd(&lh[id], 1);
-    __syncthreads();
-    if (t < 128 && lh[t] > 0)
-        gb[t] = (sv[t] - sh[t]) + atomicAdd(&cur[t * HPAD], lh[t]);
-    __syncthreads();
-    bucket[gb[id] + r] = n;
-}
-
-__global__ __launch_bounds__(256, 4)
-void k_reg(const unsigned short* __restrict__ XRB, const unsigned short* __restrict__ wbf,
-           const float* __restrict__ cm2b, const float* __restrict__ cm3w,
-           const float* __restrict__ cm3b, const int* __restrict__ hist,
-           const int* __restrict__ bucket, float* __restrict__ out)
-{
-    __shared__ __align__(16) unsigned short XP[4 * NST];
-    __shared__ float red[64];
-    __shared__ int sh[128];
-    __shared__ int sv[128];
-    __shared__ int st[128];
-    __shared__ int skj[2];
-    int bid = blockIdx.x;
-    int t = threadIdx.x;
-    if (t < 128) {
-        int h = hist[t * HPAD];
-        sh[t] = h; sv[t] = h; st[t] = (h + 63) >> 6;
-    }
-    __syncthreads();
-    for (int d = 1; d < 128; d <<= 1) {
-        int a = (t < 128 && t >= d) ? sv[t - d] : 0;
-        int b = (t < 128 && t >= d) ? st[t - d] : 0;
-        __syncthreads();
-        if (t < 128) { sv[t] += a; st[t] += b; }
-        __syncthreads();
-    }
-    if (bid >= st[127]) return;
-    if (t < 128) {
-        int ntk = (sh[t] + 63) >> 6;
-        int tb = st[t] - ntk;
-        if (bid >= tb && bid < st[t]) { skj[0] = t; skj[1] = bid - tb; }
-    }
-    __syncthreads();
-    const int k = skj[0];
-    const int start = skj[1] << 6;
-    const int cnt = sh[k];
-    const int base = sv[k] - sh[k];
-    int lane = t & 63;
-    int wv = __builtin_amdgcn_readfirstlane(t >> 6);
-    const int n16 = lane & 15;
-    const int quad = lane >> 4;
-
-    {
-        int rs = t >> 2;
-        int q = t & 3;
-        int sidx = start + rs;
-        if (sidx >= cnt) sidx = cnt - 1;
-        int n = bucket[base + sidx];
-        const uint4* src = (const uint4*)(XRB + (unsigned)n * 128u + q * 32);
-        uint4 a0 = src[0], a1 = src[1], a2 = src[2], a3 = src[3];
-        unsigned db = (rs >> 4) * NST + q * 512 + (rs & 15) * 8;
-        *(uint4*)&XP[db]       = a0;
-        *(uint4*)&XP[db + 128] = a1;
-        *(uint4*)&XP[db + 256] = a2;
-        *(uint4*)&XP[db + 384] = a3;
-    }
-    __syncthreads();
-
-    const unsigned short* wb = wbf + UW2K + (unsigned)k * 4096u;
-    bf16x8 Bf[2][4];
-    #pragma unroll
-    for (int nf = 0; nf < 2; ++nf)
-        #pragma unroll
-        for (int kt = 0; kt < 4; ++kt)
-            Bf[nf][kt] = *(const bf16x8*)&wb[(nf * 16 + n16) * 128 + kt * 32 + quad * 8];
-
-    const f32x4 vzero = {0.f, 0.f, 0.f, 0.f};
-    f32x4 acc[2];
-    acc[0] = vzero; acc[1] = vzero;
-    #pragma unroll
-    for (int kt = 0; kt < 4; ++kt) {
-        bf16x8 Af = *(const bf16x8*)&XP[wv * NST + kt * 512 + lane * 8];
-        #pragma unroll
-        for (int nf = 0; nf < 2; ++nf)
-            acc[nf] = MFMA16(Af, Bf[nf][kt], acc[nf], 0, 0, 0);
-    }
-
-    float b2a = cm2b[k * 32 + n16], b2b = cm2b[k * 32 + 16 + n16];
-    float w3a = cm3w[k * 32 + n16], w3b = cm3w[k * 32 + 16 + n16];
-    #pragma unroll
-    for (int r = 0; r < 4; ++r) {
-        float p = lrelu(acc[0][r] + b2a) * w3a
-                + lrelu(acc[1][r] + b2b) * w3b;
-        p += __shfl_xor(p, 1);
-        p += __shfl_xor(p, 2);
-        p += __shfl_xor(p, 4);
-        p += __shfl_xor(p, 8);
-        if (n16 == 0)
-            red[wv * 16 + quad * 4 + r] = p;
-    }
-    __syncthreads();
-    if (t < 64 && start + t < cnt) {
-        int n2 = bucket[base + start + t];
-        out[n2] = ((float)k + red[t] + cm3b[k]) * (1.0f / 128.0f);
+        auto& XP = U.r.XP;  auto& red = U.r.red;
+        if (t < 128) {
+            int h = hist[t * HPAD];
+            U.r.sh[t] = h; U.r.sv[t] = h; U.r.st[t] = (h + 63) >> 6;
+        }
+        __syncthreads();
+        for (int d = 1; d < 128; d <<= 1) {
+            int a = (t < 128 && t >= d) ? U.r.sv[t - d] : 0;
+            int b = (t < 128 && t >= d) ? U.r.st[t - d] : 0;
+            __syncthreads();
+            if (t < 128) { U.r.sv[t] += a; U.r.st[t] += b; }
+            __syncthreads();
+        }
+        const int ntt = U.r.st[127];
+        const int n16 = lane & 15;
+        const int quad = lane >> 4;
+
+        for (int bid2 = bid0; bid2 < ntt; bid2 += 1024) {
+            __syncthreads();
+            if (t < 128) {
+                int ntk = (U.r.sh[t] + 63) >> 6;
+                int tb = U.r.st[t] - ntk;
+                if (bid2 >= tb && bid2 < U.r.st[t]) { U.r.skj[0] = t; U.r.skj[1] = bid2 - tb; }
+            }
+            __syncthreads();
+            const int k = U.r.skj[0];
+            const int start = U.r.skj[1] << 6;
+            const int cnt2 = U.r.sh[k];
+            const int base2 = U.r.sv[k] - U.r.sh[k];
+
+            {
+                int rs = t >> 2;
+                int q = t & 3;
+                int sidx = start + rs;
+                if (sidx >= cnt2) sidx = cnt2 - 1;
+                int n = bucket[base2 + sidx];
+                const uint4* src = (const uint4*)(XRB + (unsigned)n * 128u + q * 32);
+                uint4 a0 = src[0], a1 = src[1], a2 = src[2], a3 = src[3];
+                unsigned db = (rs >> 4) * NST + q * 512 + (rs & 15) * 8;
+                *(uint4*)&XP[db]       = a0;
+                *(uint4*)&XP[db + 128] = a1;
+                *(uint4*)&XP[db + 256] = a2;
+                *(uint4*)&XP[db + 384] = a3;
+            }
+            __syncthreads();
+
+            const unsigned short* wb = wbf + UW2K + (unsigned)k * 4096u;
+            bf16x8 Bf[2][4];
+            #pragma unroll
+            for (int nf = 0; nf < 2; ++nf)
+                #pragma unroll
+                for (int kt = 0; kt < 4; ++kt)
+                    Bf[nf][kt] = *(const bf16x8*)&wb[(nf * 16 + n16) * 128 + kt * 32 + quad * 8];
+
+            const f32x4 vzero = {0.f, 0.f, 0.f, 0.f};
+            f32x4 acc2[2];
+            acc2[0] = vzero; acc2[1] = vzero;
+            #pragma unroll
+            for (int kt = 0; kt < 4; ++kt) {
+                bf16x8 Af = *(const bf16x8*)&XP[wv * NST + kt * 512 + lane * 8];
+                #pragma unroll
+                for (int nf = 0; nf < 2; ++nf)
+                    acc2[nf] = MFMA16(Af, Bf[nf][kt], acc2[nf], 0, 0, 0);
+            }
+
+            float b2a = cm2b[k * 32 + n16], b2b = cm2b[k * 32 + 16 + n16];
+            float w3a = cm3w[k * 32 + n16], w3b = cm3w[k * 32 + 16 + n16];
+            #pragma unroll
+            for (int r = 0; r < 4; ++r) {
+                float p = lrelu(acc2[0][r] + b2a) * w3a
+                        + lrelu(acc2[1][r] + b2b) * w3b;
+                p += __shfl_xor(p, 1);
+                p += __shfl_xor(p, 2);
+                p += __shfl_xor(p, 4);
+                p += __shfl_xor(p, 8);
+                if (n16 == 0)
+                    red[wv * 16 + quad * 4 + r] = p;
+            }
+            __syncthreads();
+            if (t < 64 && start + t < cnt2) {
+                int n2 = bucket[base2 + start + t];
+                out[n2] = ((float)k + red[t] + cm3b[k]) * (1.0f / 128.0f);
+            }
+        }
     }
 }
 
@@ -652,18 +670,21 @@
     int*   tiles  = fixcnt + 4;
     int*   fixlist= tiles + 1536;
     int*   bucket = fixlist + 65536;
+    int*   bar    = bucket + 65536;
+    int*   bcnt   = bar;
+    int*   broot  = bar + 32 * HPAD;
+    int*   bgen   = bar + 33 * HPAD;
     float* out = (float*)d_out;
-
-    hipLaunchKernelGGL(k_prep, dim3(256), dim3(128), 0, stream,
-                       cl1_w, cl1_b, g1, be1, mu1, va1, cl2_w, cl2_b, cl3_w, cl3_b,
-                       reg1_w, reg1_b, gr, ber, mur, var_, cm2w, ws_f, wbf, hist, cur,
-                       fixcnt);
-    hipLaunchKernelGGL(k_fused, dim3(1024), dim3(256), 0, stream,
-                       x_in, ws_f, wbf, XRB, out + 65536, inds, hist, fixcnt, fixlist);
-    hipLaunchKernelGGL(k_fix, dim3(512), dim3(256), 0, stream,
-                       x_in, ws_f, fixcnt, fixlist, inds, hist);
-    hipLaunchKernelGGL(k_scatter, dim3(256), dim3(256), 0, stream,
-                       inds, hist, cur, bucket);
-    hipLaunchKernelGGL(k_reg, dim3(1536), dim3(256), 0, stream,
-                       XRB, wbf, cm2b, cm3w, cm3b, hist, bucket, out);
+    float* out_mask_p = out + 65536;
+
+    hipMemsetAsync(bar, 0, 34 * HPAD * sizeof(int), stream);
+
+    hipLaunchKernelGGL(k_mega, dim3(1024), dim3(256), 0, stream,
+                       x_in,
+                       cl1_w, cl1_b, g1, be1, mu1, va1, cl2_w, cl2_b,
+                       cl3_w, cl3_b, reg1_w, reg1_b, gr, ber, mur, var_,
+                       cm2w, cm2b, cm3w, cm3b,
+                       ws_f, wbf, XRB, out_mask_p,
+                       inds, hist, cur, fixcnt, fixlist, bucket, out,
+                       bcnt, broot, bgen);
 }
```

Result: slower. 622.0 us (+205.0%).
